# Kernel tuning notes

Measured on AMD Instinct MI355X. Metric: run time of the kernel, lower is better.

Reference implementation:

```python
import jax, jax.numpy as jnp
import numpy as np


def _ln(x, g, b, eps=1e-5):
    m = x.mean(-1, keepdims=True)
    v = ((x - m) ** 2).mean(-1, keepdims=True)
    return (x - m) * jax.lax.rsqrt(v + eps) * g + b


def setup_inputs() -> dict:
    key = jax.random.key(0)
    ks = jax.random.split(key, 12)
    B, S, I, H, E, P, O, EM = 32, 512, 64, 512, 8, 96, 64, 512
    D = S * I
    r = lambda k, shape, s=0.02: jax.random.normal(k, shape, jnp.float32) * s
    z = lambda *shape: jnp.zeros(shape, jnp.float32)
    o = lambda *shape: jnp.ones(shape, jnp.float32)
    return dict(
        x=jax.random.normal(ks[0], (B, S, I), jnp.float32),
        gW1=r(ks[1], (D, EM)), gb1=z(EM), gln1_g=o(EM), gln1_b=z(EM),
        gW2=r(ks[2], (EM, EM)), gb2=z(EM), gln2_g=o(EM), gln2_b=z(EM),
        gW3=r(ks[3], (EM, 128)), gb3=z(128),
        protos=jax.random.normal(ks[4], (E, 128), jnp.float32) * 0.01,
        temp=jnp.ones((), jnp.float32),
        eW1=r(ks[5], (E, I, H)), eb1=z(E, H),
        eW2=r(ks[6], (E, H, H)), eb2=z(E, H),
        fW1=r(ks[7], (H, H)), fb1=z(H), fln_g=o(H), fln_b=z(H),
        fW2=r(ks[8], (H, H)), fb2=z(H),
        ln_g=o(H), ln_b=z(H),
        pW1=r(ks[9], (H, H // 2)), pb1=z(H // 2), pln_g=o(H // 2), pln_b=z(H // 2),
        pW2=r(ks[10], (H // 2, P * O)), pb2=z(P * O),
        on_g=o(O), on_b=z(O),
    )


def reference(x, gW1, gb1, gln1_g, gln1_b, gW2, gb2, gln2_g, gln2_b, gW3, gb3,
              protos, temp, eW1, eb1, eW2, eb2,
              fW1, fb1, fln_g, fln_b, fW2, fb2, ln_g, ln_b,
              pW1, pb1, pln_g, pln_b, pW2, pb2, on_g, on_b):
    B, S, I = x.shape
    O = on_g.shape[0]
    P = pW2.shape[1] // O
    # 1) flow latent mapping (identity fallback path of the original code)
    x_flat = x.reshape(B, S * I)
    z_latent = x_flat
    # 2) gating encoder -> 128-d embedding (dropout = identity in eval)
    h = jax.nn.relu(_ln(z_latent @ gW1 + gb1, gln1_g, gln1_b))
    h = jax.nn.relu(_ln(h @ gW2 + gb2, gln2_g, gln2_b))
    emb = h @ gW3 + gb3  # [B, 128]
    # 3) routing: euclidean cdist to prototypes, temperature-scaled softmax
    d2 = jnp.sum((emb[:, None, :] - protos[None, :, :]) ** 2, axis=-1)
    dist = jnp.sqrt(jnp.maximum(d2, 1e-12))  # [B, E]
    t = jnp.clip(temp, 0.1, 5.0)
    w = jax.nn.softmax(-dist / t, axis=-1)  # [B, E]
    # 4) experts: per-expert FFN on raw input, all experts batched
    he = jax.nn.relu(jnp.einsum('bsi,eih->besh', x, eW1) + eb1[None, :, None, :])
    eo = jnp.einsum('besh,eho->beso', he, eW2) + eb2[None, :, None, :]  # [B,E,S,H]
    # 5) routing-weighted combine + fusion + prediction head
    fused = jnp.einsum('besh,be->bsh', eo, w)
    f = jax.nn.relu(_ln(fused @ fW1 + fb1, fln_g, fln_b)) @ fW2 + fb2
    f = _ln(f, ln_g, ln_b)
    last = f[:, -1, :]  # [B, H]
    p = jax.nn.relu(_ln(last @ pW1 + pb1, pln_g, pln_b)) @ pW2 + pb2
    p = p.reshape(B, P, O)
    return _ln(p, on_g, on_b)
```

## Files before the change

### kernel.cpp

```cpp
#include <hip/hip_runtime.h>
#include <math.h>

#define DIMK 32768

__device__ __forceinline__ void fma4(float4& a, float s, const float4 w) {
  a.x += s * w.x; a.y += s * w.y; a.z += s * w.z; a.w += s * w.w;
}

__device__ __forceinline__ float fsel(const float4& v, int kk) {
  return kk == 0 ? v.x : kk == 1 ? v.y : kk == 2 ? v.z : v.w;
}

__device__ __forceinline__ float wave_sum(float v) {
  v += __shfl_xor(v, 1); v += __shfl_xor(v, 2); v += __shfl_xor(v, 4);
  v += __shfl_xor(v, 8); v += __shfl_xor(v, 16); v += __shfl_xor(v, 32);
  return v;
}

__device__ __forceinline__ void gld_lds16(const float* g, float* l) {
  __builtin_amdgcn_global_load_lds(
      (const __attribute__((address_space(1))) void*)g,
      (__attribute__((address_space(3))) void*)l, 16, 0, 0);
}

__device__ __forceinline__ float block_sum(float v, float* red, int n) {
  int t = threadIdx.x;
  red[t] = v;
  __syncthreads();
  for (int s = n >> 1; s > 0; s >>= 1) {
    if (t < s) red[t] += red[t + s];
    __syncthreads();
  }
  float r = red[0];
  __syncthreads();
  return r;
}

__global__ __launch_bounds__(256) void gemm1(const float* __restrict__ x,
                                             const float* __restrict__ gW1,
                                             float* __restrict__ part) {
  const int mt = blockIdx.x, ks = blockIdx.y;
  const int m0 = mt * 128, k0 = ks * 256;
  const int t = threadIdx.x;
  __shared__ float As[32 * 256];
  __shared__ float Ws[2][32 * 128];

  const float* Wp = gW1 + (size_t)k0 * 512 + m0;

#pragma unroll
  for (int j = 0; j < 8; ++j) {
    int i = t + j * 256;
    gld_lds16(x + (size_t)(i >> 6) * DIMK + k0 + (i & 63) * 4, &As[i * 4]);
  }
#pragma unroll
  for (int j = 0; j < 4; ++j) {
    int i = t + j * 256;
    gld_lds16(Wp + (size_t)(i >> 5) * 512 + (i & 31) * 4, &Ws[0][i * 4]);
  }

  const int mf4 = (t & 31) * 4;
  const int bg = t >> 5;
  float4 acc[4];
#pragma unroll
  for (int j = 0; j < 4; ++j) acc[j] = make_float4(0.f, 0.f, 0.f, 0.f);
  const float* a0 = &As[bg * 4 * 256];

  for (int s = 0; s < 8; ++s) {
    __syncthreads();
    if (s < 7) {
      const float* Wn = Wp + (size_t)(s + 1) * 32 * 512;
#pragma unroll
      for (int j = 0; j < 4; ++j) {
        int i = t + j * 256;
        gld_lds16(Wn + (size_t)(i >> 5) * 512 + (i & 31) * 4, &Ws[(s + 1) & 1][i * 4]);
      }
    }
    const float* Wc = Ws[s & 1];
    const int sc = s * 32;
#pragma unroll
    for (int kq = 0; kq < 8; ++kq) {
      float4 av0 = *(const float4*)(a0 + sc + kq * 4);
      float4 av1 = *(const float4*)(a0 + 256 + sc + kq * 4);
      float4 av2 = *(const float4*)(a0 + 512 + sc + kq * 4);
      float4 av3 = *(const float4*)(a0 + 768 + sc + kq * 4);
#pragma unroll
      for (int kk = 0; kk < 4; ++kk) {
        float4 wv = *(const float4*)&Wc[(kq * 4 + kk) * 128 + mf4];
        fma4(acc[0], fsel(av0, kk), wv);
        fma4(acc[1], fsel(av1, kk), wv);
        fma4(acc[2], fsel(av2, kk), wv);
        fma4(acc[3], fsel(av3, kk), wv);
      }
    }
  }

  float* op = part + ((size_t)ks * 32 + bg * 4) * 512 + m0 + mf4;
#pragma unroll
  for (int j = 0; j < 4; ++j) *(float4*)(op + (size_t)j * 512) = acc[j];
}

__global__ __launch_bounds__(256) void pr_he(const float* __restrict__ part,
                                             float* __restrict__ pre,
                                             const float* __restrict__ x,
                                             const float* __restrict__ eW1,
                                             const float* __restrict__ eb1,
                                             float* __restrict__ he_all) {
  __shared__ float sm[18432];
  const int bid = blockIdx.x, t = threadIdx.x;
  if (bid < 256) {
    const int b = bid & 31, c = bid >> 5;
#pragma unroll
    for (int h = 0; h < 2; ++h) {
      int m = t + h * 256;
      float a = 0.f;
      const float* p = part + ((size_t)c * 16 * 32 + b) * 512 + m;
#pragma unroll
      for (int i = 0; i < 16; ++i) a += p[(size_t)i * 16384];
      pre[((size_t)c * 32 + b) * 512 + m] = a;
    }
  } else {
    const int idx = bid - 256;
    const int e = idx >> 1, hs = idx & 1;
    float* xs = sm;
    float* Ws = sm + 2048;
    for (int i = t; i < 512; i += 256) {
      int b = i >> 4, q = i & 15;
      *(float4*)&xs[b * 64 + q * 4] = *(const float4*)(x + (size_t)b * DIMK + 32704 + q * 4);
    }
    const float* w1 = eW1 + (size_t)e * 64 * 512 + hs * 256;
    for (int i = t; i < 64 * 64; i += 256) {
      int k = i >> 6, q = i & 63;
      *(float4*)&Ws[k * 256 + q * 4] = *(const float4*)(w1 + (size_t)k * 512 + q * 4);
    }
    __syncthreads();
    float acc[32];
#pragma unroll
    for (int b = 0; b < 32; ++b) acc[b] = 0.f;
#pragma unroll 4
    for (int k = 0; k < 64; ++k) {
      float wk = Ws[k * 256 + t];
#pragma unroll
      for (int b = 0; b < 32; ++b) acc[b] += xs[b * 64 + k] * wk;
    }
    float bb = eb1[e * 512 + hs * 256 + t];
    for (int b = 0; b < 32; ++b)
      he_all[((size_t)e * 32 + b) * 512 + hs * 256 + t] = fmaxf(acc[b] + bb, 0.f);
  }
}

__global__ __launch_bounds__(256) void ln_eg(const float* __restrict__ pre,
                                             const float* __restrict__ gb1,
                                             const float* __restrict__ g,
                                             const float* __restrict__ bt,
                                             float* __restrict__ h1,
                                             const float* __restrict__ he_all,
                                             const float* __restrict__ eW2,
                                             float* __restrict__ epart) {
  __shared__ float sm[6272];
  const int bid = blockIdx.x, t = threadIdx.x;
  if (bid < 32) {
    const int b = bid;
    float a0 = gb1[t], a1 = gb1[t + 256];
    for (int kq = 0; kq < 8; ++kq) {
      const float* p = pre + ((size_t)kq * 32 + b) * 512;
      a0 += p[t]; a1 += p[t + 256];
    }
    const int lane = t & 63, wid = t >> 6;
    float s = wave_sum(a0 + a1);
    if (lane == 0) sm[wid] = s;
    __syncthreads();
    float mean = (sm[0] + sm[1] + sm[2] + sm[3]) * (1.f / 512.f);
    float d0 = a0 - mean, d1 = a1 - mean;
    __syncthreads();
    float q = wave_sum(d0 * d0 + d1 * d1);
    if (lane == 0) sm[wid] = q;
    __syncthreads();
    float var = (sm[0] + sm[1] + sm[2] + sm[3]) * (1.f / 512.f);
    float rr = rsqrtf(var + 1e-5f);
    h1[b * 512 + t] = fmaxf(d0 * rr * g[t] + bt[t], 0.f);
    h1[b * 512 + t + 256] = fmaxf(d1 * rr * g[t + 256] + bt[t + 256], 0.f);
  } else {
    const int idx = bid - 32;
    const int mt = idx & 7, kq = (idx >> 3) & 7, e = idx >> 6;
    constexpr int KC = 64;
    float* Ws = sm;
    float* As = sm + KC * 64;
    const int m0 = mt * 64, k0 = kq * KC;
    const float* Wp = eW2 + (size_t)e * 512 * 512 + (size_t)k0 * 512 + m0;
    for (int i = t; i < KC * 16; i += 256) {
      int r = i >> 4, q = i & 15;
      *(float4*)&Ws[r * 64 + q * 4] = *(const float4*)(Wp + (size_t)r * 512 + q * 4);
    }
    const float* Ap = he_all + (size_t)e * 32 * 512 + k0;
    for (int i = t; i < 32 * (KC / 4); i += 256) {
      int b = i / (KC / 4), q = i % (KC / 4);
      *(float4*)&As[b * (KC + 4) + q * 4] = *(const float4*)(Ap + (size_t)b * 512 + q * 4);
    }
    __syncthreads();
    const int mf = t & 15, bg = t >> 4;
    const int b0 = bg * 2;
    float4 acc0 = make_float4(0.f, 0.f, 0.f, 0.f), acc1 = acc0;
    const float* a0 = &As[b0 * (KC + 4)];
    const float* a1 = &As[(b0 + 1) * (KC + 4)];
#pragma unroll 8
    for (int k = 0; k < KC; ++k) {
      float4 wv = *(const float4*)&Ws[k * 64 + mf * 4];
      fma4(acc0, a0[k], wv);
      fma4(acc1, a1[k], wv);
    }
    float* op = epart + ((size_t)(kq * 8 + e) * 32 + b0) * 512 + m0 + mf * 4;
    *(float4*)op = acc0;
    *(float4*)(op + 512) = acc1;
  }
}

template <int KC>
__global__ __launch_bounds__(256) void gemm_tile(const float* __restrict__ A,
                                                 const float* __restrict__ W,
                                                 float* __restrict__ outp,
                                                 int M, int aRow) {
  const int mt = blockIdx.x, kq = blockIdx.y;
  const int m0 = mt * 64, k0 = kq * KC;
  const int t = threadIdx.x;
  __shared__ float Ws[KC * 64];
  __shared__ float As[32 * (KC + 4)];
  const float* Wp = W + (size_t)k0 * M + m0;
  for (int i = t; i < KC * 16; i += 256) {
    int r = i >> 4, q = i & 15;
    *(float4*)&Ws[r * 64 + q * 4] = *(const float4*)(Wp + (size_t)r * M + q * 4);
  }
  const float* Ap = A + k0;
  for (int i = t; i < 32 * (KC / 4); i += 256) {
    int b = i / (KC / 4), q = i % (KC / 4);
    *(float4*)&As[b * (KC + 4) + q * 4] = *(const float4*)(Ap + (size_t)b * aRow + q * 4);
  }
  __syncthreads();
  const int mf = t & 15, bg = t >> 4;
  const int b0 = bg * 2;
  float4 acc0 = make_float4(0.f, 0.f, 0.f, 0.f), acc1 = acc0;
  const float* a0 = &As[b0 * (KC + 4)];
  const float* a1 = &As[(b0 + 1) * (KC + 4)];
#pragma unroll 8
  for (int k = 0; k < KC; ++k) {
    float4 wv = *(const float4*)&Ws[k * 64 + mf * 4];
    fma4(acc0, a0[k], wv);
    fma4(acc1, a1[k], wv);
  }
  float* op = outp + ((size_t)kq * 32 + b0) * M + m0 + mf * 4;
  *(float4*)op = acc0;
  *(float4*)(op + M) = acc1;
}

__global__ void red_ln(const float* __restrict__ zp, const float* __restrict__ bias,
                       const float* __restrict__ g, const float* __restrict__ bt,
                       float* __restrict__ outp, int M, int nq, int relu) {
  const int b = blockIdx.x, t = threadIdx.x;
  __shared__ float red[512];
  float a = bias[t];
#pragma unroll 4
  for (int kq = 0; kq < nq; ++kq) a += zp[((size_t)kq * 32 + b) * M + t];
  float fM = 1.f / (float)M;
  float mean = block_sum(a, red, M) * fM;
  float d = a - mean;
  float var = block_sum(d * d, red, M) * fM;
  float v = d * rsqrtf(var + 1e-5f) * g[t] + bt[t];
  outp[b * M + t] = relu ? fmaxf(v, 0.f) : v;
}

__global__ __launch_bounds__(512) void gate_fused(const float* __restrict__ h2,
                                                  const float* __restrict__ gW3,
                                                  const float* __restrict__ gb3,
                                                  const float* __restrict__ protos,
                                                  const float* __restrict__ temp,
                                                  float* __restrict__ wgt) {
  const int b = blockIdx.x, t = threadIdx.x;
  __shared__ float Arow[512];
  __shared__ float pacc[16 * 128];
  __shared__ float emb[128];
  __shared__ float d2s[8];
  Arow[t] = h2[b * 512 + t];
  __syncthreads();
  const int m4 = (t & 31) * 4, kg = t >> 5;
  const float* Wp = gW3 + (size_t)kg * 32 * 128 + m4;
  float4 acc = make_float4(0.f, 0.f, 0.f, 0.f);
  const float* ar = &Arow[kg * 32];
#pragma unroll 8
  for (int k = 0; k < 32; ++k) {
    float4 wv = *(const float4*)(Wp + (size_t)k * 128);
    fma4(acc, ar[k], wv);
  }
  *(float4*)&pacc[kg * 128 + m4] = acc;
  __syncthreads();
  if (t < 128) {
    float a = gb3[t];
#pragma unroll
    for (int k2 = 0; k2 < 16; ++k2) a += pacc[k2 * 128 + t];
    emb[t] = a;
  }
  __syncthreads();
  const int lane = t & 63, wid = t >> 6;
  float dd0 = emb[lane] - protos[wid * 128 + lane];
  float dd1 = emb[lane + 64] - protos[wid * 128 + 64 + lane];
  float q = wave_sum(dd0 * dd0 + dd1 * dd1);
  if (lane == 0) d2s[wid] = q;
  __syncthreads();
  if (t == 0) {
    float tt = fminf(fmaxf(temp[0], 0.1f), 5.0f);
    float lg[8], mx = -1e30f;
#pragma unroll
    for (int e = 0; e < 8; ++e) {
      float dist = sqrtf(fmaxf(d2s[e], 1e-12f));
      lg[e] = -dist / tt;
      mx = fmaxf(mx, lg[e]);
    }
    float se = 0.f;
#pragma unroll
    for (int e = 0; e < 8; ++e) { lg[e] = expf(lg[e] - mx); se += lg[e]; }
#pragma unroll
    for (int e = 0; e < 8; ++e) wgt[b * 8 + e] = lg[e] / se;
  }
}

__global__ __launch_bounds__(128) void ffuse(const float* __restrict__ epart,
                                             const float* __restrict__ eb2,
                                             const float* __restrict__ wgt,
                                             float* __restrict__ fused) {
  const int b = blockIdx.x, t = blockIdx.y * 128 + threadIdx.x;
  __shared__ float wl[8];
  if (threadIdx.x < 8) wl[threadIdx.x] = wgt[b * 8 + threadIdx.x];
  __syncthreads();
  float a = 0.f;
#pragma unroll
  for (int e = 0; e < 8; ++e) {
    float s = eb2[e * 512 + t];
#pragma unroll
    for (int kq = 0; kq < 8; ++kq)
      s += epart[(((size_t)kq * 8 + e) * 32 + b) * 512 + t];
    a += wl[e] * s;
  }
  fused[b * 512 + t] = a;
}

__global__ __launch_bounds__(256) void fin_red(const float* __restrict__ fpart,
                                               const float* __restrict__ pb2,
                                               const float* __restrict__ ong,
                                               const float* __restrict__ onb,
                                               float* __restrict__ outp) {
  const int t = threadIdx.x;
  const int lane = t & 63, w = t >> 6;
  const int r = blockIdx.x * 4 + w;
  const int b = r / 96, pi = r % 96;
  const int m = pi * 64 + lane;
  float a = pb2[m];
#pragma unroll
  for (int kq = 0; kq < 4; ++kq) a += fpart[((size_t)kq * 32 + b) * 6144 + m];
  float s = wave_sum(a);
  float mean = s * (1.f / 64.f);
  float d = a - mean;
  float q = wave_sum(d * d);
  float rr = rsqrtf(q * (1.f / 64.f) + 1e-5f);
  outp[((size_t)b * 96 + pi) * 64 + lane] = d * rr * ong[lane] + onb[lane];
}

extern "C" void kernel_launch(void* const* d_in, const int* in_sizes, int n_in,
                              void* d_out, int out_size, void* d_ws, size_t ws_size,
                              hipStream_t stream) {
  (void)in_sizes; (void)n_in; (void)out_size; (void)ws_size;
  const float* x      = (const float*)d_in[0];
  const float* gW1    = (const float*)d_in[1];
  const float* gb1    = (const float*)d_in[2];
  const float* gln1_g = (const float*)d_in[3];
  const float* gln1_b = (const float*)d_in[4];
  const float* gW2    = (const float*)d_in[5];
  const float* gb2    = (const float*)d_in[6];
  const float* gln2_g = (const float*)d_in[7];
  const float* gln2_b = (const float*)d_in[8];
  const float* gW3    = (const float*)d_in[9];
  const float* gb3    = (const float*)d_in[10];
  const float* protos = (const float*)d_in[11];
  const float* temp   = (const float*)d_in[12];
  const float* eW1    = (const float*)d_in[13];
  const float* eb1    = (const float*)d_in[14];
  const float* eW2    = (const float*)d_in[15];
  const float* eb2    = (const float*)d_in[16];
  const float* fW1    = (const float*)d_in[17];
  const float* fb1    = (const float*)d_in[18];
  const float* fln_g  = (const float*)d_in[19];
  const float* fln_b  = (const float*)d_in[20];
  const float* fW2    = (const float*)d_in[21];
  const float* fb2    = (const float*)d_in[22];
  const float* ln_g   = (const float*)d_in[23];
  const float* ln_b   = (const float*)d_in[24];
  const float* pW1    = (const float*)d_in[25];
  const float* pb1    = (const float*)d_in[26];
  const float* pln_g  = (const float*)d_in[27];
  const float* pln_b  = (const float*)d_in[28];
  const float* pW2    = (const float*)d_in[29];
  const float* pb2    = (const float*)d_in[30];
  const float* on_g   = (const float*)d_in[31];
  const float* on_b   = (const float*)d_in[32];
  float* out = (float*)d_out;

  float* ws     = (float*)d_ws;
  float* part   = ws;
  float* epart  = ws;
  float* he_all = ws + 1048576;
  float* fpart  = ws;
  float* h1     = ws + 2097152;
  float* h2     = h1 + 16384;
  float* zp     = h2 + 16384;
  float* wgt    = zp + 262144;
  float* fused  = wgt + 256;
  float* f1     = fused + 16384;
  float* lastv  = f1 + 16384;
  float* pp     = lastv + 16384;

  gemm1<<<dim3(4, 128), 256, 0, stream>>>(x, gW1, part);
  pr_he<<<272, 256, 0, stream>>>(part, zp, x, eW1, eb1, he_all);
  ln_eg<<<544, 256, 0, stream>>>(zp, gb1, gln1_g, gln1_b, h1, he_all, eW2, epart);
  gemm_tile<64><<<dim3(8, 8), 256, 0, stream>>>(h1, gW2, zp, 512, 512);
  red_ln<<<32, 512, 0, stream>>>(zp, gb2, gln2_g, gln2_b, h2, 512, 8, 1);
  gate_fused<<<32, 512, 0, stream>>>(h2, gW3, gb3, protos, temp, wgt);
  ffuse<<<dim3(32, 4), 128, 0, stream>>>(epart, eb2, wgt, fused);
  gemm_tile<64><<<dim3(8, 8), 256, 0, stream>>>(fused, fW1, zp, 512, 512);
  red_ln<<<32, 512, 0, stream>>>(zp, fb1, fln_g, fln_b, f1, 512, 8, 1);
  gemm_tile<64><<<dim3(8, 8), 256, 0, stream>>>(f1, fW2, zp, 512, 512);
  red_ln<<<32, 512, 0, stream>>>(zp, fb2, ln_g, ln_b, lastv, 512, 8, 0);
  gemm_tile<64><<<dim3(4, 8), 256, 0, stream>>>(lastv, pW1, zp, 256, 512);
  red_ln<<<32, 256, 0, stream>>>(zp, pb1, pln_g, pln_b, pp, 256, 8, 1);
  gemm_tile<64><<<dim3(96, 4), 256, 0, stream>>>(pp, pW2, fpart, 6144, 256);
  fin_red<<<768, 256, 0, stream>>>(fpart, pb2, on_g, on_b, out);
}
```

Measured before the change: 265.1 us.

## Fuse gate LN/routing/expert-mix and final projection GEMM with output LayerNorm

Merges red_ln, gate_fused and ffuse into one gate_mix kernel that does the second gating LayerNorm, the embedding, the prototype softmax and the routing-weighted expert combine in a single block per batch row. The split-K pW2 GEMM and its fin_red reduction are replaced by a single pgemm_ln kernel that stages a 64-column slice of pW2 and all activations in LDS and applies the per-group LayerNorm in registers. This cuts three kernel launches and the intermediate workspace round trips. In exchange, the final GEMM runs on only 96 blocks with about 97KB of LDS each, and gate_mix serialises more work in 32 blocks.

```diff
diff --git a/kernel.cpp b/kernel.cpp
--- a/kernel.cpp
+++ b/kernel.cpp
@@ -14,6 +14,12 @@
 __device__ __forceinline__ float wave_sum(float v) {
   v += __shfl_xor(v, 1); v += __shfl_xor(v, 2); v += __shfl_xor(v, 4);
   v += __shfl_xor(v, 8); v += __shfl_xor(v, 16); v += __shfl_xor(v, 32);
+  return v;
+}
+
+__device__ __forceinline__ float group16_sum(float v) {
+  v += __shfl_xor(v, 1); v += __shfl_xor(v, 2);
+  v += __shfl_xor(v, 4); v += __shfl_xor(v, 8);
   return v;
 }
 
@@ -267,19 +273,34 @@
   outp[b * M + t] = relu ? fmaxf(v, 0.f) : v;
 }
 
-__global__ __launch_bounds__(512) void gate_fused(const float* __restrict__ h2,
-                                                  const float* __restrict__ gW3,
-                                                  const float* __restrict__ gb3,
-                                                  const float* __restrict__ protos,
-                                                  const float* __restrict__ temp,
-                                                  float* __restrict__ wgt) {
+__global__ __launch_bounds__(512) void gate_mix(const float* __restrict__ zp,
+                                                const float* __restrict__ gb2,
+                                                const float* __restrict__ g2,
+                                                const float* __restrict__ bt2,
+                                                const float* __restrict__ gW3,
+                                                const float* __restrict__ gb3,
+                                                const float* __restrict__ protos,
+                                                const float* __restrict__ temp,
+                                                const float* __restrict__ epart,
+                                                const float* __restrict__ eb2,
+                                                float* __restrict__ fused) {
   const int b = blockIdx.x, t = threadIdx.x;
+  __shared__ float red[512];
   __shared__ float Arow[512];
   __shared__ float pacc[16 * 128];
   __shared__ float emb[128];
   __shared__ float d2s[8];
-  Arow[t] = h2[b * 512 + t];
-  __syncthreads();
+  __shared__ float wl[8];
+
+  float a = gb2[t];
+#pragma unroll
+  for (int kq = 0; kq < 8; ++kq) a += zp[((size_t)kq * 32 + b) * 512 + t];
+  float mean = block_sum(a, red, 512) * (1.f / 512.f);
+  float d = a - mean;
+  float var = block_sum(d * d, red, 512) * (1.f / 512.f);
+  Arow[t] = fmaxf(d * rsqrtf(var + 1e-5f) * g2[t] + bt2[t], 0.f);
+  __syncthreads();
+
   const int m4 = (t & 31) * 4, kg = t >> 5;
   const float* Wp = gW3 + (size_t)kg * 32 * 128 + m4;
   float4 acc = make_float4(0.f, 0.f, 0.f, 0.f);
@@ -292,12 +313,13 @@
   *(float4*)&pacc[kg * 128 + m4] = acc;
   __syncthreads();
   if (t < 128) {
-    float a = gb3[t];
-#pragma unroll
-    for (int k2 = 0; k2 < 16; ++k2) a += pacc[k2 * 128 + t];
-    emb[t] = a;
-  }
-  __syncthreads();
+    float e = gb3[t];
+#pragma unroll
+    for (int k2 = 0; k2 < 16; ++k2) e += pacc[k2 * 128 + t];
+    emb[t] = e;
+  }
+  __syncthreads();
+
   const int lane = t & 63, wid = t >> 6;
   float dd0 = emb[lane] - protos[wid * 128 + lane];
   float dd1 = emb[lane + 64] - protos[wid * 128 + 64 + lane];
@@ -317,49 +339,77 @@
 #pragma unroll
     for (int e = 0; e < 8; ++e) { lg[e] = expf(lg[e] - mx); se += lg[e]; }
 #pragma unroll
-    for (int e = 0; e < 8; ++e) wgt[b * 8 + e] = lg[e] / se;
-  }
-}
-
-__global__ __launch_bounds__(128) void ffuse(const float* __restrict__ epart,
-                                             const float* __restrict__ eb2,
-                                             const float* __restrict__ wgt,
-                                             float* __restrict__ fused) {
-  const int b = blockIdx.x, t = blockIdx.y * 128 + threadIdx.x;
-  __shared__ float wl[8];
-  if (threadIdx.x < 8) wl[threadIdx.x] = wgt[b * 8 + threadIdx.x];
-  __syncthreads();
-  float a = 0.f;
+    for (int e = 0; e < 8; ++e) wl[e] = lg[e] / se;
+  }
+  __syncthreads();
+
+  float fa = 0.f;
 #pragma unroll
   for (int e = 0; e < 8; ++e) {
     float s = eb2[e * 512 + t];
 #pragma unroll
     for (int kq = 0; kq < 8; ++kq)
       s += epart[(((size_t)kq * 8 + e) * 32 + b) * 512 + t];
-    a += wl[e] * s;
-  }
-  fused[b * 512 + t] = a;
-}
-
-__global__ __launch_bounds__(256) void fin_red(const float* __restrict__ fpart,
-                                               const float* __restrict__ pb2,
-                                               const float* __restrict__ ong,
-                                               const float* __restrict__ onb,
-                                               float* __restrict__ outp) {
+    fa += wl[e] * s;
+  }
+  fused[b * 512 + t] = fa;
+}
+
+__global__ __launch_bounds__(256) void pgemm_ln(const float* __restrict__ pp,
+                                                const float* __restrict__ pW2,
+                                                const float* __restrict__ pb2,
+                                                const float* __restrict__ ong,
+                                                const float* __restrict__ onb,
+                                                float* __restrict__ outp) {
+  const int pi = blockIdx.x;
+  const int m0 = pi * 64;
   const int t = threadIdx.x;
-  const int lane = t & 63, w = t >> 6;
-  const int r = blockIdx.x * 4 + w;
-  const int b = r / 96, pi = r % 96;
-  const int m = pi * 64 + lane;
-  float a = pb2[m];
-#pragma unroll
-  for (int kq = 0; kq < 4; ++kq) a += fpart[((size_t)kq * 32 + b) * 6144 + m];
-  float s = wave_sum(a);
-  float mean = s * (1.f / 64.f);
-  float d = a - mean;
-  float q = wave_sum(d * d);
-  float rr = rsqrtf(q * (1.f / 64.f) + 1e-5f);
-  outp[((size_t)b * 96 + pi) * 64 + lane] = d * rr * ong[lane] + onb[lane];
+  __shared__ float Ws[256 * 64];
+  __shared__ float As[32 * 260];
+  const float* Wp = pW2 + m0;
+  for (int i = t; i < 4096; i += 256) {
+    int r = i >> 4, q = i & 15;
+    *(float4*)&Ws[r * 64 + q * 4] = *(const float4*)(Wp + (size_t)r * 6144 + q * 4);
+  }
+  for (int i = t; i < 2048; i += 256) {
+    int b = i >> 6, q = i & 63;
+    *(float4*)&As[b * 260 + q * 4] = *(const float4*)(pp + (size_t)b * 256 + q * 4);
+  }
+  __syncthreads();
+  const int mf = t & 15, bg = t >> 4;
+  const int b0 = bg * 2;
+  float4 acc0 = make_float4(0.f, 0.f, 0.f, 0.f), acc1 = acc0;
+  const float* a0 = &As[b0 * 260];
+  const float* a1 = &As[(b0 + 1) * 260];
+#pragma unroll 8
+  for (int k = 0; k < 256; ++k) {
+    float4 wv = *(const float4*)&Ws[k * 64 + mf * 4];
+    fma4(acc0, a0[k], wv);
+    fma4(acc1, a1[k], wv);
+  }
+  const float4 pbv = *(const float4*)(pb2 + m0 + mf * 4);
+  const float4 gv = *(const float4*)(ong + mf * 4);
+  const float4 bv = *(const float4*)(onb + mf * 4);
+  acc0.x += pbv.x; acc0.y += pbv.y; acc0.z += pbv.z; acc0.w += pbv.w;
+  acc1.x += pbv.x; acc1.y += pbv.y; acc1.z += pbv.z; acc1.w += pbv.w;
+
+  float s0 = group16_sum(acc0.x + acc0.y + acc0.z + acc0.w);
+  float mean0 = s0 * (1.f / 64.f);
+  float4 d0 = make_float4(acc0.x - mean0, acc0.y - mean0, acc0.z - mean0, acc0.w - mean0);
+  float q0 = group16_sum(d0.x * d0.x + d0.y * d0.y + d0.z * d0.z + d0.w * d0.w);
+  float rr0 = rsqrtf(q0 * (1.f / 64.f) + 1e-5f);
+  float4 o0 = make_float4(d0.x * rr0 * gv.x + bv.x, d0.y * rr0 * gv.y + bv.y,
+                          d0.z * rr0 * gv.z + bv.z, d0.w * rr0 * gv.w + bv.w);
+  float s1 = group16_sum(acc1.x + acc1.y + acc1.z + acc1.w);
+  float mean1 = s1 * (1.f / 64.f);
+  float4 d1 = make_float4(acc1.x - mean1, acc1.y - mean1, acc1.z - mean1, acc1.w - mean1);
+  float q1 = group16_sum(d1.x * d1.x + d1.y * d1.y + d1.z * d1.z + d1.w * d1.w);
+  float rr1 = rsqrtf(q1 * (1.f / 64.f) + 1e-5f);
+  float4 o1 = make_float4(d1.x * rr1 * gv.x + bv.x, d1.y * rr1 * gv.y + bv.y,
+                          d1.z * rr1 * gv.z + bv.z, d1.w * rr1 * gv.w + bv.w);
+
+  *(float4*)(outp + ((size_t)b0 * 96 + pi) * 64 + mf * 4) = o0;
+  *(float4*)(outp + ((size_t)(b0 + 1) * 96 + pi) * 64 + mf * 4) = o1;
 }
 
 extern "C" void kernel_launch(void* const* d_in, const int* in_sizes, int n_in,
@@ -405,12 +455,9 @@
   float* part   = ws;
   float* epart  = ws;
   float* he_all = ws + 1048576;
-  float* fpart  = ws;
   float* h1     = ws + 2097152;
-  float* h2     = h1 + 16384;
-  float* zp     = h2 + 16384;
-  float* wgt    = zp + 262144;
-  float* fused  = wgt + 256;
+  float* zp     = h1 + 16384;
+  float* fused  = zp + 262144;
   float* f1     = fused + 16384;
   float* lastv  = f1 + 16384;
   float* pp     = lastv + 16384;
@@ -419,15 +466,13 @@
   pr_he<<<272, 256, 0, stream>>>(part, zp, x, eW1, eb1, he_all);
   ln_eg<<<544, 256, 0, stream>>>(zp, gb1, gln1_g, gln1_b, h1, he_all, eW2, epart);
   gemm_tile<64><<<dim3(8, 8), 256, 0, stream>>>(h1, gW2, zp, 512, 512);
-  red_ln<<<32, 512, 0, stream>>>(zp, gb2, gln2_g, gln2_b, h2, 512, 8, 1);
-  gate_fused<<<32, 512, 0, stream>>>(h2, gW3, gb3, protos, temp, wgt);
-  ffuse<<<dim3(32, 4), 128, 0, stream>>>(epart, eb2, wgt, fused);
+  gate_mix<<<32, 512, 0, stream>>>(zp, gb2, gln2_g, gln2_b, gW3, gb3, protos,
+                                   temp, epart, eb2, fused);
   gemm_tile<64><<<dim3(8, 8), 256, 0, stream>>>(fused, fW1, zp, 512, 512);
   red_ln<<<32, 512, 0, stream>>>(zp, fb1, fln_g, fln_b, f1, 512, 8, 1);
   gemm_tile<64><<<dim3(8, 8), 256, 0, stream>>>(f1, fW2, zp, 512, 512);
   red_ln<<<32, 512, 0, stream>>>(zp, fb2, ln_g, ln_b, lastv, 512, 8, 0);
   gemm_tile<64><<<dim3(4, 8), 256, 0, stream>>>(lastv, pW1, zp, 256, 512);
   red_ln<<<32, 256, 0, stream>>>(zp, pb1, pln_g, pln_b, pp, 256, 8, 1);
-  gemm_tile<64><<<dim3(96, 4), 256, 0, stream>>>(pp, pW2, fpart, 6144, 256);
-  fin_red<<<768, 256, 0, stream>>>(fpart, pb2, on_g, on_b, out);
-}
+  pgemm_ln<<<96, 256, 0, stream>>>(pp, pW2, pb2, on_g, on_b, out);
+}
```

After: 280.8 us. 5.9% more time.
